# Kernel optimization log

Hardware: AMD Instinct MI355X
Metric: run time of the kernel (lower is better)

Reference implementation:

```python
import jax, jax.numpy as jnp
import numpy as np
from functools import partial

N_FIXED, B, L, T, K = 64, 5000, 10, 25, 8
N = 1_000_000


def setup_inputs() -> dict:
    key = jax.random.key(0)
    ks = jax.random.split(key, 8)
    X = jax.random.normal(ks[0], (N, N_FIXED), dtype=jnp.float32)
    batter_ids = jax.random.randint(ks[1], (N,), 0, B)
    league_ids = jax.random.randint(ks[2], (N,), 0, L)
    season_ids = jax.random.randint(ks[3], (N,), 0, T)
    # learned parameters (match torch init: beta=0, raw_rho=0 -> use small noise
    # for a non-degenerate reference; Sigma = identity per head K)
    beta = jax.random.normal(ks[4], (N_FIXED, K), dtype=jnp.float32) * 0.02
    raw_rho = jax.random.normal(ks[5], (L, K), dtype=jnp.float32) * 0.1
    Sigma = jnp.tile(jnp.eye(L, dtype=jnp.float32)[None], (K, 1, 1))
    eps = jax.random.normal(ks[6], (B, L, T, K), dtype=jnp.float32)
    return {"X": X, "batter_ids": batter_ids, "league_ids": league_ids,
            "season_ids": season_ids, "beta": beta, "raw_rho": raw_rho,
            "Sigma": Sigma, "eps": eps}


def _random_effects(raw_rho, Sigma, eps):
    # SigmaHalf: (K,L,L); torch einsum 'KLL,BLK->BLK' repeats L -> diagonal only
    SigmaHalf = jnp.linalg.cholesky(Sigma)
    d = jnp.diagonal(SigmaHalf, axis1=1, axis2=2).T      # (L,K)
    rho = jnp.tanh(raw_rho)                              # (L,K)
    e = jnp.transpose(eps, (2, 0, 1, 3))                 # (T,B,L,K)
    u0 = e[0]                                            # u_0 = eps_0 (no scaling)

    def step(u_prev, eps_t):
        u = rho * u_prev + d * eps_t
        return u, u

    _, us = jax.lax.scan(step, u0, e[1:])                # (T-1,B,L,K)
    return jnp.concatenate([u0[None], us], axis=0)       # (T,B,L,K)


def reference(X, batter_ids, league_ids, season_ids, beta, raw_rho, Sigma, eps):
    fixed = X @ beta                                     # (n,K)
    u = _random_effects(raw_rho, Sigma, eps)             # (T,B,L,K)
    rand = u[season_ids, batter_ids, league_ids, :]      # (n,K) gather
    return fixed + rand
```

## Files before the change

kernel.cpp:

```cpp
#include <hip/hip_runtime.h>
#include <math.h>

#define NROWS 1000000
#define NF    64
#define BB    5000
#define LLg   10
#define TTg   25
#define KKg   8

#define WS_RHO   0
#define WS_D     80
#define WS_U     1024

__global__ void prep_kernel(const float* __restrict__ raw_rho,
                            const float* __restrict__ Sigma,
                            float* __restrict__ ws) {
    const int tid = threadIdx.x;
    for (int i = tid; i < LLg * KKg; i += blockDim.x)
        ws[WS_RHO + i] = tanhf(raw_rho[i]);
    if (tid < KKg) {
        const int k = tid;
        float Lf[LLg][LLg];
        const float* S = Sigma + k * LLg * LLg;
        for (int i = 0; i < LLg; ++i) {
            for (int j = 0; j <= i; ++j) {
                float s = S[i * LLg + j];
                for (int m = 0; m < j; ++m) s -= Lf[i][m] * Lf[j][m];
                if (i == j) Lf[i][i] = sqrtf(s);
                else        Lf[i][j] = s / Lf[j][j];
            }
        }
        for (int l = 0; l < LLg; ++l)
            ws[WS_D + l * KKg + k] = Lf[l][l];
    }
}

__global__ __launch_bounds__(256) void u_kernel(const float* __restrict__ eps,
                                                const float* __restrict__ ws,
                                                float* __restrict__ u) {
    const int tid = blockIdx.x * blockDim.x + threadIdx.x;
    if (tid >= BB * LLg * KKg) return;
    const int k = tid % KKg;
    const int l = (tid / KKg) % LLg;
    const int b = tid / (KKg * LLg);
    const float rho = ws[WS_RHO + l * KKg + k];
    const float dv  = ws[WS_D   + l * KKg + k];
    const float* ep = eps + ((size_t)(b * LLg + l) * TTg) * KKg + k;
    float* up = u + (size_t)(b * LLg + l) * KKg + k;
    const size_t ustride = (size_t)BB * LLg * KKg;
    float uv = ep[0];
    up[0] = uv;
    for (int t = 1; t < TTg; ++t) {
        uv = rho * uv + dv * ep[(size_t)t * KKg];
        up[(size_t)t * ustride] = uv;
    }
}

template <bool USE_TABLE>
__global__ __launch_bounds__(256) void main_kernel(
    const float* __restrict__ X,
    const int*   __restrict__ bat,
    const int*   __restrict__ lea,
    const int*   __restrict__ sea,
    const float* __restrict__ beta,
    const float* __restrict__ ws,
    const float* __restrict__ u_table,
    const float* __restrict__ eps,
    float*       __restrict__ out)
{
    __shared__ float sbeta[8 * 68];
    for (int i = threadIdx.x; i < NF * KKg; i += blockDim.x) {
        const int f = i >> 3, k = i & 7;
        sbeta[(f >> 3) * 68 + (f & 7) * 8 + k] = beta[i];
    }
    __syncthreads();

    const int gt   = blockIdx.x * blockDim.x + threadIdx.x;
    const int j    = gt & 7;
    const int g    = gt >> 3;
    const int row0 = g * 2;

    const int2 bb = *(const int2*)(bat + row0);
    const int2 ll = *(const int2*)(lea + row0);
    const int2 tt = *(const int2*)(sea + row0);

    const float* xr0p = X + (size_t)row0 * NF + j * 8;
    const float* xr1p = X + (size_t)(row0 + 1) * NF + j * 8;
    float xr0[8], xr1[8];
    *(float4*)&xr0[0] = ((const float4*)xr0p)[0];
    *(float4*)&xr0[4] = ((const float4*)xr0p)[1];
    *(float4*)&xr1[0] = ((const float4*)xr1p)[0];
    *(float4*)&xr1[4] = ((const float4*)xr1p)[1];

    float uv0, uv1;
    if (USE_TABLE) {
        uv0 = u_table[(((size_t)tt.x * BB + bb.x) * LLg + ll.x) * KKg + j];
        uv1 = u_table[(((size_t)tt.y * BB + bb.y) * LLg + ll.y) * KKg + j];
    } else {
        const float rho0 = ws[WS_RHO + ll.x * KKg + j];
        const float dv0  = ws[WS_D   + ll.x * KKg + j];
        const float* e0  = eps + ((size_t)(bb.x * LLg + ll.x) * TTg) * KKg + j;
        uv0 = e0[0];
        for (int s = 1; s <= tt.x; ++s) uv0 = rho0 * uv0 + dv0 * e0[(size_t)s * KKg];
        const float rho1 = ws[WS_RHO + ll.y * KKg + j];
        const float dv1  = ws[WS_D   + ll.y * KKg + j];
        const float* e1  = eps + ((size_t)(bb.y * LLg + ll.y) * TTg) * KKg + j;
        uv1 = e1[0];
        for (int s = 1; s <= tt.y; ++s) uv1 = rho1 * uv1 + dv1 * e1[(size_t)s * KKg];
    }

    float bv[8][8];
#pragma unroll
    for (int ff = 0; ff < 8; ++ff) {
        const float4* p = (const float4*)&sbeta[j * 68 + ff * 8];
        const float4 u0 = p[0], u1 = p[1];
        bv[ff][0] = u0.x; bv[ff][1] = u0.y; bv[ff][2] = u0.z; bv[ff][3] = u0.w;
        bv[ff][4] = u1.x; bv[ff][5] = u1.y; bv[ff][6] = u1.z; bv[ff][7] = u1.w;
    }

    float p0[8], p1[8];
#pragma unroll
    for (int k = 0; k < 8; ++k) { p0[k] = 0.f; p1[k] = 0.f; }
#pragma unroll
    for (int ff = 0; ff < 8; ++ff) {
#pragma unroll
        for (int k = 0; k < 8; ++k) {
            p0[k] += xr0[ff] * bv[ff][k];
            p1[k] += xr1[ff] * bv[ff][k];
        }
    }

#pragma unroll
    for (int i = 0; i < 4; ++i) {
        const float s0 = (j & 4) ? p0[i] : p0[i + 4];
        const float s1 = (j & 4) ? p1[i] : p1[i + 4];
        const float k0 = (j & 4) ? p0[i + 4] : p0[i];
        const float k1 = (j & 4) ? p1[i + 4] : p1[i];
        p0[i] = k0 + __shfl_xor(s0, 4);
        p1[i] = k1 + __shfl_xor(s1, 4);
    }
#pragma unroll
    for (int i = 0; i < 2; ++i) {
        const float s0 = (j & 2) ? p0[i] : p0[i + 2];
        const float s1 = (j & 2) ? p1[i] : p1[i + 2];
        const float k0 = (j & 2) ? p0[i + 2] : p0[i];
        const float k1 = (j & 2) ? p1[i + 2] : p1[i];
        p0[i] = k0 + __shfl_xor(s0, 2);
        p1[i] = k1 + __shfl_xor(s1, 2);
    }
    {
        const float s0 = (j & 1) ? p0[0] : p0[1];
        const float s1 = (j & 1) ? p1[0] : p1[1];
        const float k0 = (j & 1) ? p0[1] : p0[0];
        const float k1 = (j & 1) ? p1[1] : p1[0];
        p0[0] = k0 + __shfl_xor(s0, 1);
        p1[0] = k1 + __shfl_xor(s1, 1);
    }

    out[(size_t)row0 * KKg + j]       = p0[0] + uv0;
    out[(size_t)(row0 + 1) * KKg + j] = p1[0] + uv1;
}

extern "C" void kernel_launch(void* const* d_in, const int* in_sizes, int n_in,
                              void* d_out, int out_size, void* d_ws, size_t ws_size,
                              hipStream_t stream) {
    const float* X       = (const float*)d_in[0];
    const int*   bat     = (const int*)  d_in[1];
    const int*   lea     = (const int*)  d_in[2];
    const int*   sea     = (const int*)  d_in[3];
    const float* beta    = (const float*)d_in[4];
    const float* raw_rho = (const float*)d_in[5];
    const float* Sigma   = (const float*)d_in[6];
    const float* eps     = (const float*)d_in[7];
    float* out = (float*)d_out;
    float* ws  = (float*)d_ws;
    float* u   = ws + WS_U;

    const size_t need_bytes = ((size_t)WS_U + (size_t)TTg * BB * LLg * KKg) * sizeof(float);
    const bool use_table = ws_size >= need_bytes;

    prep_kernel<<<1, 128, 0, stream>>>(raw_rho, Sigma, ws);

    const int nthreads = (NROWS / 2) * KKg;
    const int nblocks  = nthreads / 256;

    if (use_table) {
        u_kernel<<<(BB * LLg * KKg + 255) / 256, 256, 0, stream>>>(eps, ws, u);
        main_kernel<true><<<nblocks, 256, 0, stream>>>(X, bat, lea, sea, beta, ws, u, eps, out);
    } else {
        main_kernel<false><<<nblocks, 256, 0, stream>>>(X, bat, lea, sea, beta, ws, u, eps, out);
    }
}
```

Measured before the change: 400.9 us.

## Fold prep into per-block LDS setup, add nontemporal loads/stores, preload eps

Removes the separate single-block prep kernel launch: each block now computes tanh(rho) and the Cholesky diagonal into shared memory itself. The streaming X, id arrays and output use nontemporal loads/stores so they do not pollute cache, keeping the gathered u table more cache-resident. u_kernel preloads all 25 eps values before the recurrence. Cost is redundant Cholesky work in every u_kernel block (8 threads serial) and more register pressure.

```diff
diff --git a/kernel.cpp b/kernel.cpp
--- a/kernel.cpp
+++ b/kernel.cpp
@@ -8,50 +8,70 @@
 #define TTg   25
 #define KKg   8
 
-#define WS_RHO   0
-#define WS_D     80
-#define WS_U     1024
-
-__global__ void prep_kernel(const float* __restrict__ raw_rho,
-                            const float* __restrict__ Sigma,
-                            float* __restrict__ ws) {
+#define WS_U 1024
+
+typedef float f32x4 __attribute__((ext_vector_type(4)));
+typedef int   i32x2 __attribute__((ext_vector_type(2)));
+
+__device__ __forceinline__ void prep_lds(const float* __restrict__ raw_rho,
+                                         const float* __restrict__ Sigma,
+                                         float* s_rho, float* s_d,
+                                         float (*s_L)[55]) {
     const int tid = threadIdx.x;
-    for (int i = tid; i < LLg * KKg; i += blockDim.x)
-        ws[WS_RHO + i] = tanhf(raw_rho[i]);
+    if (tid < LLg * KKg) s_rho[tid] = tanhf(raw_rho[tid]);
     if (tid < KKg) {
         const int k = tid;
-        float Lf[LLg][LLg];
         const float* S = Sigma + k * LLg * LLg;
+        float* Lt = s_L[k];
         for (int i = 0; i < LLg; ++i) {
+            const int ib = i * (i + 1) / 2;
             for (int j = 0; j <= i; ++j) {
+                const int jb = j * (j + 1) / 2;
                 float s = S[i * LLg + j];
-                for (int m = 0; m < j; ++m) s -= Lf[i][m] * Lf[j][m];
-                if (i == j) Lf[i][i] = sqrtf(s);
-                else        Lf[i][j] = s / Lf[j][j];
+                for (int m = 0; m < j; ++m) s -= Lt[ib + m] * Lt[jb + m];
+                if (i == j) {
+                    const float v = sqrtf(s);
+                    Lt[ib + j] = v;
+                    s_d[i * KKg + k] = v;
+                } else {
+                    Lt[ib + j] = s / Lt[jb + j];
+                }
             }
         }
-        for (int l = 0; l < LLg; ++l)
-            ws[WS_D + l * KKg + k] = Lf[l][l];
     }
 }
 
 __global__ __launch_bounds__(256) void u_kernel(const float* __restrict__ eps,
-                                                const float* __restrict__ ws,
+                                                const float* __restrict__ raw_rho,
+                                                const float* __restrict__ Sigma,
                                                 float* __restrict__ u) {
+    __shared__ float s_rho[LLg * KKg];
+    __shared__ float s_d[LLg * KKg];
+    __shared__ float s_L[KKg][55];
+    prep_lds(raw_rho, Sigma, s_rho, s_d, s_L);
+    __syncthreads();
+
     const int tid = blockIdx.x * blockDim.x + threadIdx.x;
     if (tid >= BB * LLg * KKg) return;
     const int k = tid % KKg;
     const int l = (tid / KKg) % LLg;
     const int b = tid / (KKg * LLg);
-    const float rho = ws[WS_RHO + l * KKg + k];
-    const float dv  = ws[WS_D   + l * KKg + k];
+    const float rho = s_rho[l * KKg + k];
+    const float dv  = s_d[l * KKg + k];
     const float* ep = eps + ((size_t)(b * LLg + l) * TTg) * KKg + k;
     float* up = u + (size_t)(b * LLg + l) * KKg + k;
     const size_t ustride = (size_t)BB * LLg * KKg;
-    float uv = ep[0];
+
+    float ev[TTg];
+#pragma unroll
+    for (int t = 0; t < TTg; ++t)
+        ev[t] = __builtin_nontemporal_load(ep + (size_t)t * KKg);
+
+    float uv = ev[0];
     up[0] = uv;
+#pragma unroll
     for (int t = 1; t < TTg; ++t) {
-        uv = rho * uv + dv * ep[(size_t)t * KKg];
+        uv = rho * uv + dv * ev[t];
         up[(size_t)t * ustride] = uv;
     }
 }
@@ -63,12 +83,20 @@
     const int*   __restrict__ lea,
     const int*   __restrict__ sea,
     const float* __restrict__ beta,
-    const float* __restrict__ ws,
     const float* __restrict__ u_table,
+    const float* __restrict__ raw_rho,
+    const float* __restrict__ Sigma,
     const float* __restrict__ eps,
     float*       __restrict__ out)
 {
     __shared__ float sbeta[8 * 68];
+    __shared__ float s_rho[LLg * KKg];
+    __shared__ float s_d[LLg * KKg];
+    __shared__ float s_L[KKg][55];
+
+    if (!USE_TABLE)
+        prep_lds(raw_rho, Sigma, s_rho, s_d, s_L);
+
     for (int i = threadIdx.x; i < NF * KKg; i += blockDim.x) {
         const int f = i >> 3, k = i & 7;
         sbeta[(f >> 3) * 68 + (f & 7) * 8 + k] = beta[i];
@@ -80,30 +108,35 @@
     const int g    = gt >> 3;
     const int row0 = g * 2;
 
-    const int2 bb = *(const int2*)(bat + row0);
-    const int2 ll = *(const int2*)(lea + row0);
-    const int2 tt = *(const int2*)(sea + row0);
+    const i32x2 bb = __builtin_nontemporal_load((const i32x2*)(bat + row0));
+    const i32x2 ll = __builtin_nontemporal_load((const i32x2*)(lea + row0));
+    const i32x2 tt = __builtin_nontemporal_load((const i32x2*)(sea + row0));
 
     const float* xr0p = X + (size_t)row0 * NF + j * 8;
     const float* xr1p = X + (size_t)(row0 + 1) * NF + j * 8;
+    const f32x4 x0a = __builtin_nontemporal_load((const f32x4*)xr0p);
+    const f32x4 x0b = __builtin_nontemporal_load((const f32x4*)xr0p + 1);
+    const f32x4 x1a = __builtin_nontemporal_load((const f32x4*)xr1p);
+    const f32x4 x1b = __builtin_nontemporal_load((const f32x4*)xr1p + 1);
     float xr0[8], xr1[8];
-    *(float4*)&xr0[0] = ((const float4*)xr0p)[0];
-    *(float4*)&xr0[4] = ((const float4*)xr0p)[1];
-    *(float4*)&xr1[0] = ((const float4*)xr1p)[0];
-    *(float4*)&xr1[4] = ((const float4*)xr1p)[1];
+#pragma unroll
+    for (int i = 0; i < 4; ++i) {
+        xr0[i] = x0a[i]; xr0[i + 4] = x0b[i];
+        xr1[i] = x1a[i]; xr1[i + 4] = x1b[i];
+    }
 
     float uv0, uv1;
     if (USE_TABLE) {
         uv0 = u_table[(((size_t)tt.x * BB + bb.x) * LLg + ll.x) * KKg + j];
         uv1 = u_table[(((size_t)tt.y * BB + bb.y) * LLg + ll.y) * KKg + j];
     } else {
-        const float rho0 = ws[WS_RHO + ll.x * KKg + j];
-        const float dv0  = ws[WS_D   + ll.x * KKg + j];
+        const float rho0 = s_rho[ll.x * KKg + j];
+        const float dv0  = s_d[ll.x * KKg + j];
         const float* e0  = eps + ((size_t)(bb.x * LLg + ll.x) * TTg) * KKg + j;
         uv0 = e0[0];
         for (int s = 1; s <= tt.x; ++s) uv0 = rho0 * uv0 + dv0 * e0[(size_t)s * KKg];
-        const float rho1 = ws[WS_RHO + ll.y * KKg + j];
-        const float dv1  = ws[WS_D   + ll.y * KKg + j];
+        const float rho1 = s_rho[ll.y * KKg + j];
+        const float dv1  = s_d[ll.y * KKg + j];
         const float* e1  = eps + ((size_t)(bb.y * LLg + ll.y) * TTg) * KKg + j;
         uv1 = e1[0];
         for (int s = 1; s <= tt.y; ++s) uv1 = rho1 * uv1 + dv1 * e1[(size_t)s * KKg];
@@ -157,8 +190,8 @@
         p1[0] = k1 + __shfl_xor(s1, 1);
     }
 
-    out[(size_t)row0 * KKg + j]       = p0[0] + uv0;
-    out[(size_t)(row0 + 1) * KKg + j] = p1[0] + uv1;
+    __builtin_nontemporal_store(p0[0] + uv0, out + (size_t)row0 * KKg + j);
+    __builtin_nontemporal_store(p1[0] + uv1, out + (size_t)(row0 + 1) * KKg + j);
 }
 
 extern "C" void kernel_launch(void* const* d_in, const int* in_sizes, int n_in,
@@ -179,15 +212,15 @@
     const size_t need_bytes = ((size_t)WS_U + (size_t)TTg * BB * LLg * KKg) * sizeof(float);
     const bool use_table = ws_size >= need_bytes;
 
-    prep_kernel<<<1, 128, 0, stream>>>(raw_rho, Sigma, ws);
-
     const int nthreads = (NROWS / 2) * KKg;
     const int nblocks  = nthreads / 256;
 
     if (use_table) {
-        u_kernel<<<(BB * LLg * KKg + 255) / 256, 256, 0, stream>>>(eps, ws, u);
-        main_kernel<true><<<nblocks, 256, 0, stream>>>(X, bat, lea, sea, beta, ws, u, eps, out);
+        u_kernel<<<(BB * LLg * KKg + 255) / 256, 256, 0, stream>>>(eps, raw_rho, Sigma, u);
+        main_kernel<true><<<nblocks, 256, 0, stream>>>(X, bat, lea, sea, beta, u,
+                                                       raw_rho, Sigma, eps, out);
     } else {
-        main_kernel<false><<<nblocks, 256, 0, stream>>>(X, bat, lea, sea, beta, ws, u, eps, out);
-    }
-}
+        main_kernel<false><<<nblocks, 256, 0, stream>>>(X, bat, lea, sea, beta, u,
+                                                        raw_rho, Sigma, eps, out);
+    }
+}
```

Result: no change. 400.7 us (-0.1%).
